# Kernel optimization log

Measured on AMD Instinct MI355X. Metric: run time of the kernel, lower is better.

The kernel has to match this reference:

```python
import jax, jax.numpy as jnp
import numpy as np

N_NODES = 100000
N_EDGES = 1600000
NUM_FEATURES = 128
HIDDEN = 64
NUM_CLASSES = 2


def _gcn_norm(edge_index, num_nodes):
    # PyG gcn_norm: add self-loops, symmetric degree normalization.
    loop = jnp.arange(num_nodes, dtype=edge_index.dtype)
    src = jnp.concatenate([edge_index[0], loop])
    dst = jnp.concatenate([edge_index[1], loop])
    deg = jax.ops.segment_sum(jnp.ones_like(src, dtype=jnp.float32), dst,
                              num_segments=num_nodes)
    dinv = jnp.where(deg > 0, jax.lax.rsqrt(deg), 0.0)
    norm = dinv[src] * dinv[dst]  # [E + N]
    return src, dst, norm


def _gcn_conv(x, src, dst, norm, W, b, num_nodes):
    h = x @ W  # linear transform first (PyG GCNConv)
    msg = h[src] * norm[:, None]  # gather + edge scaling, [E+N, H]
    out = jax.ops.segment_sum(msg, dst, num_segments=num_nodes)  # scatter-add
    return out + b


def setup_inputs() -> dict:
    key = jax.random.key(0)
    ks = jax.random.split(key, 8)
    x = jax.random.normal(ks[0], (N_NODES, NUM_FEATURES), dtype=jnp.float32)
    edge_index = jax.random.randint(ks[1], (2, N_EDGES), 0, N_NODES, dtype=jnp.int32)
    def glorot(k, shape):
        lim = np.sqrt(6.0 / (shape[0] + shape[1]))
        return jax.random.uniform(k, shape, jnp.float32, -lim, lim)
    return {
        "x": x,
        "edge_index": edge_index,
        "W1": glorot(ks[2], (NUM_FEATURES, HIDDEN)),
        "b1": jnp.zeros((HIDDEN,), jnp.float32),
        "W2": glorot(ks[3], (HIDDEN, HIDDEN)),
        "b2": jnp.zeros((HIDDEN,), jnp.float32),
        "W3": glorot(ks[4], (HIDDEN, HIDDEN)),
        "b3": jnp.zeros((HIDDEN,), jnp.float32),
        "Wlin": glorot(ks[5], (HIDDEN, NUM_CLASSES)),
        "blin": jnp.zeros((NUM_CLASSES,), jnp.float32),
    }


def reference(x, edge_index, W1, b1, W2, b2, W3, b3, Wlin, blin):
    num_nodes = x.shape[0]
    src, dst, norm = _gcn_norm(edge_index, num_nodes)
    # eval mode: dropout is identity
    h = jax.nn.relu(_gcn_conv(x, src, dst, norm, W1, b1, num_nodes))
    h = jax.nn.relu(_gcn_conv(h, src, dst, norm, W2, b2, num_nodes))
    h = jax.nn.relu(_gcn_conv(h, src, dst, norm, W3, b3, num_nodes))
    logits = h @ Wlin + blin
    return jax.nn.log_softmax(logits, axis=1)
```

## Files before the change

kernel.cpp:

```cpp
#include <hip/hip_runtime.h>
#include <cstdint>
#include <cstddef>

#define NF 128
#define NH 64

typedef unsigned int uint32;
typedef short bf16x8 __attribute__((ext_vector_type(8)));
typedef float f32x4 __attribute__((ext_vector_type(4)));

__device__ inline unsigned short f2bf(float f) {
  unsigned int u = __float_as_uint(f);
  return (unsigned short)((u + 0x7FFF + ((u >> 16) & 1)) >> 16);
}
__device__ inline float bf2f_lo(uint32 u) { return __uint_as_float(u << 16); }
__device__ inline float bf2f_hi(uint32 u) { return __uint_as_float(u & 0xFFFF0000u); }


__global__ __launch_bounds__(256) void gemm1_count_kernel(
    const float* __restrict__ X, const float* __restrict__ W,
    uint32* __restrict__ Hb, int N,
    const int* __restrict__ ei, int E, int* __restrict__ cnt, int RW, int G1) {
  if ((int)blockIdx.x >= G1) {
    int b = blockIdx.x - G1;
    int pass = b & 1;
    int i = (b >> 1) * 256 + threadIdx.x;
    if (i * 4 >= E) return;
    int4 d = ((const int4*)(ei + E))[i];
    int lo = pass * RW, hi = lo + RW;
    if (d.x >= lo && d.x < hi) atomicAdd(&cnt[d.x], 1);
    if (d.y >= lo && d.y < hi) atomicAdd(&cnt[d.y], 1);
    if (d.z >= lo && d.z < hi) atomicAdd(&cnt[d.z], 1);
    if (d.w >= lo && d.w < hi) atomicAdd(&cnt[d.w], 1);
    return;
  }

  const int lane = threadIdx.x & 63;
  const int wv = threadIdx.x >> 6;
  const int m = lane & 15;
  const int g = lane >> 4;
  const int base = blockIdx.x * 64 + wv * 16;
  int row = base + m;
  int rowc = row < N ? row : N - 1;
  const float* xp = X + (size_t)rowc * 128 + g * 8;

  f32x4 acc[4];
#pragma unroll
  for (int nt = 0; nt < 4; ++nt) acc[nt] = (f32x4){0.f, 0.f, 0.f, 0.f};

#pragma unroll
  for (int kk = 0; kk < 4; ++kk) {
    float4 alo = *(const float4*)(xp + kk * 32);
    float4 ahi = *(const float4*)(xp + kk * 32 + 4);
    bf16x8 a;
    a[0] = (short)f2bf(alo.x); a[1] = (short)f2bf(alo.y);
    a[2] = (short)f2bf(alo.z); a[3] = (short)f2bf(alo.w);
    a[4] = (short)f2bf(ahi.x); a[5] = (short)f2bf(ahi.y);
    a[6] = (short)f2bf(ahi.z); a[7] = (short)f2bf(ahi.w);
    const float* wp = W + (size_t)(kk * 32 + g * 8) * 64 + m;
#pragma unroll
    for (int nt = 0; nt < 4; ++nt) {
      bf16x8 b;
#pragma unroll
      for (int i = 0; i < 8; ++i)
        b[i] = (short)f2bf(wp[(size_t)i * 64 + nt * 16]);
      acc[nt] = __builtin_amdgcn_mfma_f32_16x16x32_bf16(a, b, acc[nt], 0, 0, 0);
    }
  }
  unsigned short* Hs = (unsigned short*)Hb;
#pragma unroll
  for (int j = 0; j < 4; ++j) {
    int n = base + g * 4 + j;
    if (n < N) {
#pragma unroll
      for (int nt = 0; nt < 4; ++nt)
        Hs[(size_t)n * 64 + nt * 16 + m] = f2bf(acc[nt][j]);
    }
  }
}

__global__ __launch_bounds__(256) void partial_kernel(const int* __restrict__ cnt, int N,
                                                      int* __restrict__ part) {
  __shared__ int sd[256];
  int t = threadIdx.x;
  int idx = blockIdx.x * 1024 + t * 4;
  int s = 0;
#pragma unroll
  for (int j = 0; j < 4; ++j)
    if (idx + j < N) s += cnt[idx + j];
  sd[t] = s;
  __syncthreads();
  for (int off = 128; off > 0; off >>= 1) {
    if (t < off) sd[t] += sd[t + off];
    __syncthreads();
  }
  if (t == 0) part[blockIdx.x] = sd[0];
}

__global__ __launch_bounds__(128) void scanp_kernel(int* __restrict__ part, int NB,
                                                    int* __restrict__ rowptrN) {
  __shared__ int s[128];
  int t = threadIdx.x;
  int v = (t < NB) ? part[t] : 0;
  s[t] = v;
  __syncthreads();
  for (int off = 1; off < 128; off <<= 1) {
    int add = (t >= off) ? s[t - off] : 0;
    __syncthreads();
    s[t] += add;
    __syncthreads();
  }
  if (t < NB) part[t] = s[t] - v;
  if (t == 0) rowptrN[0] = s[127];
}

__global__ __launch_bounds__(256) void rowptr_kernel(const int* __restrict__ cnt,
                                                     const int* __restrict__ part,
                                                     int* __restrict__ rowptr,
                                                     int* __restrict__ cnt2,
                                                     float* __restrict__ dinv, int N) {
  __shared__ int s[256];
  int t = threadIdx.x;
  int idx = blockIdx.x * 1024 + t * 4;
  int c[4];
  int ts = 0;
#pragma unroll
  for (int j = 0; j < 4; ++j) {
    c[j] = (idx + j < N) ? cnt[idx + j] : 0;
    ts += c[j];
  }
  s[t] = ts;
  __syncthreads();
  for (int off = 1; off < 256; off <<= 1) {
    int add = (t >= off) ? s[t - off] : 0;
    __syncthreads();
    s[t] += add;
    __syncthreads();
  }
  int run = s[t] - ts + part[blockIdx.x];
#pragma unroll
  for (int j = 0; j < 4; ++j) {
    if (idx + j < N) {
      rowptr[idx + j] = run;
      cnt2[idx + j] = run;
      dinv[idx + j] = rsqrtf((float)(c[j] + 1));
    }
    run += c[j];
  }
}

__global__ __launch_bounds__(256) void fill_kernel(const int* __restrict__ ei, int E,
                                                   int* __restrict__ cnt2,
                                                   const float* __restrict__ dinv,
                                                   int2* __restrict__ col2, int RW) {
  int pass = blockIdx.x & 3;
  int i = (blockIdx.x >> 2) * 256 + threadIdx.x;
  if (i * 4 >= E) return;
  int4 sv = ((const int4*)ei)[i];
  int4 dv = ((const int4*)(ei + E))[i];
  int lo = pass * RW, hi = lo + RW;
  int ss[4] = {sv.x, sv.y, sv.z, sv.w};
  int dd[4] = {dv.x, dv.y, dv.z, dv.w};
#pragma unroll
  for (int j = 0; j < 4; ++j) {
    int d = dd[j];
    if (d < lo || d >= hi) continue;
    int s = ss[j];
    float w = dinv[s] * dinv[d];
    int pos = atomicAdd(&cnt2[d], 1);
    col2[pos] = make_int2(s, __float_as_int(w));
  }
}


template <int FINAL>
__global__ __launch_bounds__(256) void prop_fused_kernel(
    const uint32* __restrict__ H32, const int* __restrict__ rowptr,
    const int2* __restrict__ col2, const float* __restrict__ dinv,
    const float* __restrict__ bias, const float* __restrict__ Wn,
    const float* __restrict__ blin, void* __restrict__ outv, int N) {
  __shared__ float Ws[FINAL ? 4 : 64 * 64];
  __shared__ float rbuf[FINAL ? 1 : 4][64];
  const int lane = threadIdx.x & 63;
  const int widx = threadIdx.x >> 6;
  const int fl = lane & 31;
  const int half = lane >> 5;

  if (!FINAL) {
    const float4* Wg = (const float4*)Wn;
    float4* Wl = (float4*)Ws;
    for (int i = threadIdx.x; i < 1024; i += 256) Wl[i] = Wg[i];
    __syncthreads();
  }

  int n = blockIdx.x * 4 + widx;
  n = __builtin_amdgcn_readfirstlane(n);
  if (n >= N) return;

  int e0 = rowptr[n];
  int e1 = rowptr[n + 1];
  float di = dinv[n];
  const int2* ec = col2 + e0;
  const int m = e1 - e0;

  float acc0 = 0.f, acc1 = 0.f;
  if (half == 0) {
    uint32 u = H32[(size_t)n * 32 + fl];
    float w = di * di;
    acc0 = bf2f_lo(u) * w;
    acc1 = bf2f_hi(u) * w;
  }

  const int npair = m >> 1;
  const int nfull = npair >> 3;
  for (int b = 0; b < nfull; ++b) {
    int s[8];
    float wv[8];
#pragma unroll
    for (int j = 0; j < 8; ++j) {
      int2 c = ec[2 * (b * 8 + j) + half];
      s[j] = c.x;
      wv[j] = __int_as_float(c.y);
    }
    uint32 u[8];
#pragma unroll
    for (int j = 0; j < 8; ++j) u[j] = H32[(size_t)s[j] * 32 + fl];
#pragma unroll
    for (int j = 0; j < 8; ++j) {
      acc0 = fmaf(wv[j], bf2f_lo(u[j]), acc0);
      acc1 = fmaf(wv[j], bf2f_hi(u[j]), acc1);
    }
  }
  for (int t = nfull * 8; t < npair; ++t) {
    int2 c = ec[2 * t + half];
    uint32 u = H32[(size_t)c.x * 32 + fl];
    float w = __int_as_float(c.y);
    acc0 = fmaf(w, bf2f_lo(u), acc0);
    acc1 = fmaf(w, bf2f_hi(u), acc1);
  }
  if ((m & 1) && half == 0) {
    int2 c = ec[m - 1];
    uint32 u = H32[(size_t)c.x * 32 + fl];
    float w = __int_as_float(c.y);
    acc0 = fmaf(w, bf2f_lo(u), acc0);
    acc1 = fmaf(w, bf2f_hi(u), acc1);
  }
  acc0 += __shfl_xor(acc0, 32, 64);
  acc1 += __shfl_xor(acc1, 32, 64);

  float2 bv = ((const float2*)bias)[fl];
  float r0 = acc0 + bv.x;
  float r1 = acc1 + bv.y;
  r0 = r0 > 0.f ? r0 : 0.f;
  r1 = r1 > 0.f ? r1 : 0.f;

  if (FINAL) {
    float t0 = 0.f, t1 = 0.f;
    if (half == 0) {
      t0 = r0 * Wn[4 * fl + 0] + r1 * Wn[4 * fl + 2];
      t1 = r0 * Wn[4 * fl + 1] + r1 * Wn[4 * fl + 3];
    }
#pragma unroll
    for (int off = 32; off > 0; off >>= 1) {
      t0 += __shfl_xor(t0, off, 64);
      t1 += __shfl_xor(t1, off, 64);
    }
    if (lane == 0) {
      float* out = (float*)outv;
      float l0 = t0 + blin[0];
      float l1 = t1 + blin[1];
      float mx = fmaxf(l0, l1);
      float lz = mx + logf(expf(l0 - mx) + expf(l1 - mx));
      out[(size_t)n * 2 + 0] = l0 - lz;
      out[(size_t)n * 2 + 1] = l1 - lz;
    }
  } else {
    if (half == 0) *(float2*)(&rbuf[widx][2 * fl]) = make_float2(r0, r1);
    __builtin_amdgcn_wave_barrier();
    float o = 0.f;
#pragma unroll
    for (int q = 0; q < 16; ++q) {
      float4 rv = *(const float4*)(&rbuf[widx][4 * q]);
      o = fmaf(rv.x, Ws[(4 * q + 0) * 64 + lane], o);
      o = fmaf(rv.y, Ws[(4 * q + 1) * 64 + lane], o);
      o = fmaf(rv.z, Ws[(4 * q + 2) * 64 + lane], o);
      o = fmaf(rv.w, Ws[(4 * q + 3) * 64 + lane], o);
    }
    ((unsigned short*)outv)[(size_t)n * 64 + lane] = f2bf(o);
  }
}


extern "C" void kernel_launch(void* const* d_in, const int* in_sizes, int n_in,
                              void* d_out, int out_size, void* d_ws, size_t ws_size,
                              hipStream_t stream) {
  const float* x  = (const float*)d_in[0];
  const int*   ei = (const int*)d_in[1];
  const float* W1 = (const float*)d_in[2];
  const float* b1 = (const float*)d_in[3];
  const float* W2 = (const float*)d_in[4];
  const float* b2 = (const float*)d_in[5];
  const float* W3 = (const float*)d_in[6];
  const float* b3 = (const float*)d_in[7];
  const float* Wl = (const float*)d_in[8];
  const float* bl = (const float*)d_in[9];
  float* out = (float*)d_out;

  const int N = in_sizes[0] / NF;
  const int E = in_sizes[1] / 2;

  char* w = (char*)d_ws;
  size_t off = 0;
  auto alloc = [&](size_t bytes) {
    void* p = w + off;
    off += bytes;
    off = (off + 15) & ~(size_t)15;
    return p;
  };
  int*    cnt    = (int*)alloc((size_t)N * 4);
  int*    cnt2   = (int*)alloc((size_t)N * 4);
  int*    rowptr = (int*)alloc((size_t)(N + 1) * 4);
  int*    part   = (int*)alloc(256 * 4);
  float*  dinv   = (float*)alloc((size_t)N * 4);
  int2*   col2   = (int2*)alloc((size_t)E * 8);
  uint32* hA     = (uint32*)alloc((size_t)N * 32 * 4);
  uint32* hB     = (uint32*)alloc((size_t)N * 32 * 4);

  const int NB = (N + 1023) / 1024;
  const int RW2 = (N + 1) / 2;
  const int RW4 = (N + 3) / 4;
  const int NCHUNK = (E / 4 + 255) / 256;
  const int G1 = ((((N + 63) / 64) + 1) / 2) * 2;
  const int NBH = (N + 3) / 4;

  hipMemsetAsync(cnt, 0, (size_t)N * 4, stream);
  hipLaunchKernelGGL(gemm1_count_kernel, dim3(G1 + 2 * NCHUNK), dim3(256), 0, stream,
                     x, W1, hA, N, ei, E, cnt, RW2, G1);
  hipLaunchKernelGGL(partial_kernel, dim3(NB), dim3(256), 0, stream, cnt, N, part);
  hipLaunchKernelGGL(scanp_kernel, dim3(1), dim3(128), 0, stream, part, NB, rowptr + N);
  hipLaunchKernelGGL(rowptr_kernel, dim3(NB), dim3(256), 0, stream,
                     cnt, part, rowptr, cnt2, dinv, N);
  hipLaunchKernelGGL(fill_kernel, dim3(4 * NCHUNK), dim3(256), 0, stream,
                     ei, E, cnt2, dinv, col2, RW4);

  hipLaunchKernelGGL(prop_fused_kernel<0>, dim3(NBH), dim3(256), 0, stream,
                     hA, rowptr, col2, dinv, b1, W2, (const float*)nullptr, (void*)hB, N);
  hipLaunchKernelGGL(prop_fused_kernel<0>, dim3(NBH), dim3(256), 0, stream,
                     hB, rowptr, col2, dinv, b2, W3, (const float*)nullptr, (void*)hA, N);
  hipLaunchKernelGGL(prop_fused_kernel<1>, dim3(NBH), dim3(256), 0, stream,
                     hA, rowptr, col2, dinv, b3, Wl, bl, (void*)out, N);
}
```

Before: 420.7 us.

## Bucket CSR edges by source range within each row for gather locality

Counts and fill offsets are now kept per (destination, source-bucket) pair, with source buckets of 16384 nodes, so each row's edge list is grouped by source range. The aim is to make the feature gathers in the three propagation passes more cache-local, since concurrent warps touch similar source regions. In exchange the count and cursor arrays grow eightfold, the scan kernels read more data, and the count pass must also read source indices.

New measurement: 418.6 us. Within noise of the previous version (-0.5%).

```diff
diff --git a/kernel.cpp b/kernel.cpp
--- a/kernel.cpp
+++ b/kernel.cpp
@@ -4,6 +4,8 @@
 
 #define NF 128
 #define NH 64
+#define TSH 14
+#define NT8 8
 
 typedef unsigned int uint32;
 typedef short bf16x8 __attribute__((ext_vector_type(8)));
@@ -26,12 +28,13 @@
     int pass = b & 1;
     int i = (b >> 1) * 256 + threadIdx.x;
     if (i * 4 >= E) return;
-    int4 d = ((const int4*)(ei + E))[i];
+    int4 s4 = ((const int4*)ei)[i];
+    int4 d4 = ((const int4*)(ei + E))[i];
     int lo = pass * RW, hi = lo + RW;
-    if (d.x >= lo && d.x < hi) atomicAdd(&cnt[d.x], 1);
-    if (d.y >= lo && d.y < hi) atomicAdd(&cnt[d.y], 1);
-    if (d.z >= lo && d.z < hi) atomicAdd(&cnt[d.z], 1);
-    if (d.w >= lo && d.w < hi) atomicAdd(&cnt[d.w], 1);
+    if (d4.x >= lo && d4.x < hi) atomicAdd(&cnt[d4.x * NT8 + (s4.x >> TSH)], 1);
+    if (d4.y >= lo && d4.y < hi) atomicAdd(&cnt[d4.y * NT8 + (s4.y >> TSH)], 1);
+    if (d4.z >= lo && d4.z < hi) atomicAdd(&cnt[d4.z * NT8 + (s4.z >> TSH)], 1);
+    if (d4.w >= lo && d4.w < hi) atomicAdd(&cnt[d4.w * NT8 + (s4.w >> TSH)], 1);
     return;
   }
 
@@ -86,8 +89,13 @@
   int idx = blockIdx.x * 1024 + t * 4;
   int s = 0;
 #pragma unroll
-  for (int j = 0; j < 4; ++j)
-    if (idx + j < N) s += cnt[idx + j];
+  for (int j = 0; j < 4; ++j) {
+    if (idx + j < N) {
+      int4 a = ((const int4*)cnt)[(idx + j) * 2];
+      int4 b = ((const int4*)cnt)[(idx + j) * 2 + 1];
+      s += a.x + a.y + a.z + a.w + b.x + b.y + b.z + b.w;
+    }
+  }
   sd[t] = s;
   __syncthreads();
   for (int off = 128; off > 0; off >>= 1) {
@@ -117,17 +125,29 @@
 __global__ __launch_bounds__(256) void rowptr_kernel(const int* __restrict__ cnt,
                                                      const int* __restrict__ part,
                                                      int* __restrict__ rowptr,
-                                                     int* __restrict__ cnt2,
+                                                     int* __restrict__ cur,
                                                      float* __restrict__ dinv, int N) {
   __shared__ int s[256];
   int t = threadIdx.x;
   int idx = blockIdx.x * 1024 + t * 4;
+  int cc[4][8];
   int c[4];
   int ts = 0;
 #pragma unroll
   for (int j = 0; j < 4; ++j) {
-    c[j] = (idx + j < N) ? cnt[idx + j] : 0;
-    ts += c[j];
+    int sum = 0;
+    if (idx + j < N) {
+      int4 a = ((const int4*)cnt)[(idx + j) * 2];
+      int4 b = ((const int4*)cnt)[(idx + j) * 2 + 1];
+      cc[j][0] = a.x; cc[j][1] = a.y; cc[j][2] = a.z; cc[j][3] = a.w;
+      cc[j][4] = b.x; cc[j][5] = b.y; cc[j][6] = b.z; cc[j][7] = b.w;
+      sum = a.x + a.y + a.z + a.w + b.x + b.y + b.z + b.w;
+    } else {
+#pragma unroll
+      for (int q = 0; q < 8; ++q) cc[j][q] = 0;
+    }
+    c[j] = sum;
+    ts += sum;
   }
   s[t] = ts;
   __syncthreads();
@@ -142,7 +162,12 @@
   for (int j = 0; j < 4; ++j) {
     if (idx + j < N) {
       rowptr[idx + j] = run;
-      cnt2[idx + j] = run;
+      int cum = run;
+#pragma unroll
+      for (int q = 0; q < 8; ++q) {
+        cur[(idx + j) * NT8 + q] = cum;
+        cum += cc[j][q];
+      }
       dinv[idx + j] = rsqrtf((float)(c[j] + 1));
     }
     run += c[j];
@@ -150,7 +175,7 @@
 }
 
 __global__ __launch_bounds__(256) void fill_kernel(const int* __restrict__ ei, int E,
-                                                   int* __restrict__ cnt2,
+                                                   int* __restrict__ cur,
                                                    const float* __restrict__ dinv,
                                                    int2* __restrict__ col2, int RW) {
   int pass = blockIdx.x & 3;
@@ -167,7 +192,7 @@
     if (d < lo || d >= hi) continue;
     int s = ss[j];
     float w = dinv[s] * dinv[d];
-    int pos = atomicAdd(&cnt2[d], 1);
+    int pos = atomicAdd(&cur[d * NT8 + (s >> TSH)], 1);
     col2[pos] = make_int2(s, __float_as_int(w));
   }
 }
@@ -317,8 +342,8 @@
     off = (off + 15) & ~(size_t)15;
     return p;
   };
-  int*    cnt    = (int*)alloc((size_t)N * 4);
-  int*    cnt2   = (int*)alloc((size_t)N * 4);
+  int*    cnt    = (int*)alloc((size_t)N * NT8 * 4);
+  int*    cur    = (int*)alloc((size_t)N * NT8 * 4);
   int*    rowptr = (int*)alloc((size_t)(N + 1) * 4);
   int*    part   = (int*)alloc(256 * 4);
   float*  dinv   = (float*)alloc((size_t)N * 4);
@@ -333,15 +358,15 @@
   const int G1 = ((((N + 63) / 64) + 1) / 2) * 2;
   const int NBH = (N + 3) / 4;
 
-  hipMemsetAsync(cnt, 0, (size_t)N * 4, stream);
+  hipMemsetAsync(cnt, 0, (size_t)N * NT8 * 4, stream);
   hipLaunchKernelGGL(gemm1_count_kernel, dim3(G1 + 2 * NCHUNK), dim3(256), 0, stream,
                      x, W1, hA, N, ei, E, cnt, RW2, G1);
   hipLaunchKernelGGL(partial_kernel, dim3(NB), dim3(256), 0, stream, cnt, N, part);
   hipLaunchKernelGGL(scanp_kernel, dim3(1), dim3(128), 0, stream, part, NB, rowptr + N);
   hipLaunchKernelGGL(rowptr_kernel, dim3(NB), dim3(256), 0, stream,
-                     cnt, part, rowptr, cnt2, dinv, N);
+                     cnt, part, rowptr, cur, dinv, N);
   hipLaunchKernelGGL(fill_kernel, dim3(4 * NCHUNK), dim3(256), 0, stream,
-                     ei, E, cnt2, dinv, col2, RW4);
+                     ei, E, cur, dinv, col2, RW4);
 
   hipLaunchKernelGGL(prop_fused_kernel<0>, dim3(NBH), dim3(256), 0, stream,
                      hA, rowptr, col2, dinv, b1, W2, (const float*)nullptr, (void*)hB, N);
```
